# Kernel optimization log

Measured on AMD Instinct MI355X. Metric: run time of the kernel, lower is better.

## Reference

```python
import jax, jax.numpy as jnp
import numpy as np

NUM_NODES = 50000
NUM_HYPEREDGES = 10000
NUM_INCIDENCES = 800000
CHANNELS = 256
NEG_SLOPE = 0.01  # torch leaky_relu default negative_slope


def setup_inputs() -> dict:
    key = jax.random.key(0)
    k_n, k_e, k_emb, k_cw, k_lw, k_lb = jax.random.split(key, 6)
    node_idx = jax.random.randint(k_n, (NUM_INCIDENCES,), 0, NUM_NODES, dtype=jnp.int32)
    edge_idx = jax.random.randint(k_e, (NUM_INCIDENCES,), 0, NUM_HYPEREDGES, dtype=jnp.int32)
    edge_index = jnp.stack([node_idx, edge_idx], axis=0)  # [2, nnz] incidence list
    s = 1.0 / np.sqrt(CHANNELS).astype(np.float32)
    emb = jax.random.normal(k_emb, (NUM_NODES, CHANNELS), jnp.float32)  # Node2Vec embedding table
    conv_w = jax.random.normal(k_cw, (CHANNELS, CHANNELS), jnp.float32) * s  # HypergraphConv.lin (no bias)
    conv_b = jnp.zeros((CHANNELS,), jnp.float32)  # HypergraphConv.bias
    lin_w = jax.random.normal(k_lw, (CHANNELS, CHANNELS), jnp.float32) * s
    lin_b = jax.random.normal(k_lb, (CHANNELS,), jnp.float32) * s
    return {"emb": emb, "conv_w": conv_w, "conv_b": conv_b,
            "lin_w": lin_w, "lin_b": lin_b, "edge_index": edge_index}


def reference(emb, conv_w, conv_b, lin_w, lin_b, edge_index):
    node_idx, edge_idx = edge_index[0], edge_index[1]
    # HypergraphConv (use_attention=False): X' = D^-1 H B^-1 H^T (X W^T) + b
    x = emb @ conv_w.T  # [N, C]
    ones = jnp.ones((NUM_INCIDENCES,), x.dtype)
    D = jax.ops.segment_sum(ones, node_idx, num_segments=NUM_NODES)       # node degree
    Dinv = jnp.where(D > 0, 1.0 / D, 0.0)
    B = jax.ops.segment_sum(ones, edge_idx, num_segments=NUM_HYPEREDGES)  # hyperedge degree
    Binv = jnp.where(B > 0, 1.0 / B, 0.0)
    # node -> hyperedge aggregation
    e = jax.ops.segment_sum(x[node_idx], edge_idx, num_segments=NUM_HYPEREDGES) * Binv[:, None]  # [E, C]
    # hyperedge -> node aggregation
    n = jax.ops.segment_sum(e[edge_idx], node_idx, num_segments=NUM_NODES) * Dinv[:, None] + conv_b  # [N, C]
    y = jax.nn.leaky_relu(n, NEG_SLOPE)
    g = y.T @ y  # [C, C] Gram
    out = jax.nn.leaky_relu(g @ lin_w.T + lin_b, NEG_SLOPE)
    return out
```

## Files before the change

### kernel.cpp

```cpp
#include <hip/hip_runtime.h>

#define N_NODES 50000
#define N_EDGES 10000
#define NNZ     800000
#define C       256
#define SLOPE   0.01f
#define KTOT    50176
#define KCHUNK  512
#define NZB     98
#define MPAD    10048

#define NB      250
#define EB_E    40
#define EB_N    200
#define CHUNK   3125
#define CAP     6000
#define MP_E    288
#define MP_N    1408

#define EAGG_G  628
#define NAGG_G  1568

#define OFF_CC_E    0
#define OFF_CC_N    1024
#define OFF_CUR_E   2048
#define OFF_CUR_N   3072
#define OFF_DEG_E   4096
#define OFF_DEG_N   45056
#define ZERO_BYTES  245760
#define OFF_CB_E    266240
#define OFF_CB_N    267264
#define OFF_RS_N    268288
#define OFF_RS_E    468480
#define OFF_BUF_E   508672
#define OFF_BUF_N   3708672
#define OFF_CSR_E   6908672
#define OFF_CSR_N   10108672
#define OFF_EMBH    13308672
#define OFF_YT      13308672
#define OFF_EACC    39000064
#define OFF_E2      44144640
#define OFF_CWH     49289216
#define OFF_PART    49420288

typedef __attribute__((ext_vector_type(8))) short short8;
typedef __attribute__((ext_vector_type(4))) float floatx4;

static __device__ __forceinline__ unsigned short f2bf(float f) {
    unsigned int u = __float_as_uint(f);
    u = (u + 0x7fffu + ((u >> 16) & 1u)) >> 16;
    return (unsigned short)u;
}

static __device__ __forceinline__ void acc_bf8(const uint4 d, float* a) {
    a[0] += __uint_as_float(d.x << 16);
    a[1] += __uint_as_float(d.x & 0xffff0000u);
    a[2] += __uint_as_float(d.y << 16);
    a[3] += __uint_as_float(d.y & 0xffff0000u);
    a[4] += __uint_as_float(d.z << 16);
    a[5] += __uint_as_float(d.z & 0xffff0000u);
    a[6] += __uint_as_float(d.w << 16);
    a[7] += __uint_as_float(d.w & 0xffff0000u);
}

static __device__ __forceinline__ void idx8(const uint4 pk, int* ix) {
    ix[0] = (int)(pk.x & 0xffffu); ix[1] = (int)(pk.x >> 16);
    ix[2] = (int)(pk.y & 0xffffu); ix[3] = (int)(pk.y >> 16);
    ix[4] = (int)(pk.z & 0xffffu); ix[5] = (int)(pk.z >> 16);
    ix[6] = (int)(pk.w & 0xffffu); ix[7] = (int)(pk.w >> 16);
}

__global__ __launch_bounds__(256) void zero_kernel(float4* __restrict__ p, int n4) {
    int i = blockIdx.x * 256 + threadIdx.x;
    if (i < n4) p[i] = make_float4(0.f, 0.f, 0.f, 0.f);
}

#define PREP_EMB_BLOCKS 6251
#define PREP_CW_BLOCKS  32
__global__ __launch_bounds__(256) void prep_kernel(const float4* __restrict__ emb4,
                                                   uint4* __restrict__ embh4,
                                                   const float4* __restrict__ cw4,
                                                   uint4* __restrict__ cwh4,
                                                   const int* __restrict__ node_idx,
                                                   const int* __restrict__ edge_idx,
                                                   int* __restrict__ cc_e,
                                                   int* __restrict__ cc_n) {
    __shared__ int he[NB], hn[NB];
    int b = blockIdx.x, tid = threadIdx.x;
    if (b < PREP_EMB_BLOCKS) {
        int i = b * 256 + tid;
        if (i >= 1600032) return;
        uint4 o = {0u, 0u, 0u, 0u};
        if (i < 1600000) {
            float4 f0 = emb4[2 * i], f1 = emb4[2 * i + 1];
            o.x = f2bf(f0.x) | ((unsigned)f2bf(f0.y) << 16);
            o.y = f2bf(f0.z) | ((unsigned)f2bf(f0.w) << 16);
            o.z = f2bf(f1.x) | ((unsigned)f2bf(f1.y) << 16);
            o.w = f2bf(f1.z) | ((unsigned)f2bf(f1.w) << 16);
        }
        int node = i >> 5, c = i & 31;
        embh4[(size_t)(((c >> 2) * 50001 + node) << 2) + (c & 3)] = o;
    } else if (b < PREP_EMB_BLOCKS + PREP_CW_BLOCKS) {
        int i = (b - PREP_EMB_BLOCKS) * 256 + tid;
        float4 f0 = cw4[2 * i], f1 = cw4[2 * i + 1];
        uint4 o;
        o.x = f2bf(f0.x) | ((unsigned)f2bf(f0.y) << 16);
        o.y = f2bf(f0.z) | ((unsigned)f2bf(f0.w) << 16);
        o.z = f2bf(f1.x) | ((unsigned)f2bf(f1.y) << 16);
        o.w = f2bf(f1.z) | ((unsigned)f2bf(f1.w) << 16);
        cwh4[i] = o;
    } else {
        int base = (b - PREP_EMB_BLOCKS - PREP_CW_BLOCKS) * CHUNK;
        for (int i = tid; i < NB; i += 256) { he[i] = 0; hn[i] = 0; }
        __syncthreads();
        for (int i = tid; i < CHUNK; i += 256) {
            atomicAdd(&he[edge_idx[base + i] / EB_E], 1);
            atomicAdd(&hn[node_idx[base + i] / EB_N], 1);
        }
        __syncthreads();
        for (int k = tid; k < NB; k += 256) {
            if (he[k]) atomicAdd(&cc_e[k], he[k]);
            if (hn[k]) atomicAdd(&cc_n[k], hn[k]);
        }
    }
}

__global__ __launch_bounds__(256) void coarse_scan_kernel(const int* __restrict__ cc_e,
                                                          const int* __restrict__ cc_n,
                                                          int* __restrict__ cb_e,
                                                          int* __restrict__ cb_n) {
    __shared__ int tmp[256];
    int tid = threadIdx.x;
    int v = (tid < NB) ? cc_e[tid] : 0;
    tmp[tid] = v;
    __syncthreads();
    for (int off = 1; off < 256; off <<= 1) {
        int t = (tid >= off) ? tmp[tid - off] : 0;
        __syncthreads();
        tmp[tid] += t;
        __syncthreads();
    }
    if (tid < NB) cb_e[tid + 1] = tmp[tid];
    if (tid == 0) cb_e[0] = 0;
    __syncthreads();
    v = (tid < NB) ? cc_n[tid] : 0;
    tmp[tid] = v;
    __syncthreads();
    for (int off = 1; off < 256; off <<= 1) {
        int t = (tid >= off) ? tmp[tid - off] : 0;
        __syncthreads();
        tmp[tid] += t;
        __syncthreads();
    }
    if (tid < NB) cb_n[tid + 1] = tmp[tid];
    if (tid == 0) cb_n[0] = 0;
}

__global__ __launch_bounds__(256) void bucket_scatter_kernel(const int* __restrict__ node_idx,
                                                             const int* __restrict__ edge_idx,
                                                             const int* __restrict__ cb_e,
                                                             const int* __restrict__ cb_n,
                                                             int* __restrict__ cur_e,
                                                             int* __restrict__ cur_n,
                                                             int* __restrict__ buf_e,
                                                             int* __restrict__ buf_n) {
    __shared__ int he[NB], hn[NB], be[NB], bn[NB];
    int tid = threadIdx.x;
    int base = blockIdx.x * CHUNK;
    for (int i = tid; i < NB; i += 256) { he[i] = 0; hn[i] = 0; }
    __syncthreads();
    int pe[13], pn[13];
    #pragma unroll
    for (int k = 0; k < 13; k++) {
        int i = tid + k * 256;
        if (i < CHUNK) {
            int e = edge_idx[base + i], v = node_idx[base + i];
            int ke = e / EB_E, kn = v / EB_N;
            pe[k] = (ke << 12) | atomicAdd(&he[ke], 1);
            pn[k] = (kn << 12) | atomicAdd(&hn[kn], 1);
        }
    }
    __syncthreads();
    for (int k = tid; k < NB; k += 256) {
        int c = he[k];
        be[k] = cb_e[k] + (c ? atomicAdd(&cur_e[k], c) : 0);
        int cn = hn[k];
        bn[k] = cb_n[k] + (cn ? atomicAdd(&cur_n[k], cn) : 0);
    }
    __syncthreads();
    #pragma unroll
    for (int k = 0; k < 13; k++) {
        int i = tid + k * 256;
        if (i < CHUNK) {
            int e = edge_idx[base + i], v = node_idx[base + i];
            int ke = pe[k] >> 12, oe = pe[k] & 4095;
            buf_e[be[ke] + oe] = (v << 6) | (e - ke * EB_E);
            int kn = pn[k] >> 12, on = pn[k] & 4095;
            buf_n[bn[kn] + on] = (e << 8) | (v - kn * EB_N);
        }
    }
}

__global__ __launch_bounds__(256) void bucket_sort_kernel(const int* __restrict__ buf_e,
                                                          const int* __restrict__ buf_n,
                                                          const int* __restrict__ cb_e,
                                                          const int* __restrict__ cb_n,
                                                          unsigned short* __restrict__ csr_e,
                                                          unsigned short* __restrict__ csr_n,
                                                          int* __restrict__ rs_e,
                                                          int* __restrict__ rs_n,
                                                          int* __restrict__ deg_e,
                                                          int* __restrict__ deg_n) {
    __shared__ int A[CAP];
    __shared__ int h[EB_N], bs[EB_N], cs[EB_N];
    int tid = threadIdx.x;
    bool edgeSide = blockIdx.x < NB;
    int k = edgeSide ? blockIdx.x : blockIdx.x - NB;
    int eb = edgeSide ? EB_E : EB_N;
    int shift = edgeSide ? 6 : 8;
    int mask = (1 << shift) - 1;
    int mp = edgeSide ? MP_E : MP_N;
    int sent = edgeSide ? N_NODES : N_EDGES;
    const int* cb  = edgeSide ? cb_e : cb_n;
    const int* buf = edgeSide ? buf_e : buf_n;
    unsigned short* csr = edgeSide ? csr_e : csr_n;
    int* rs  = edgeSide ? rs_e : rs_n;
    int* deg = edgeSide ? deg_e : deg_n;
    int base = cb[k];
    int base_pad = (base + k * mp + 7) & ~7;
    int cnt = cb[k + 1] - base;
    for (int i = tid; i < eb; i += 256) h[i] = 0;
    __syncthreads();
    for (int i = tid; i < cnt; i += 256) {
        int it = buf[base + i];
        if (i < CAP) A[i] = it;
        atomicAdd(&h[it & mask], 1);
    }
    __syncthreads();
    if (tid == 0) {
        int s = 0;
        for (int j = 0; j < eb; j++) { bs[j] = s; s += (h[j] + 7) & ~7; }
    }
    __syncthreads();
    for (int j = tid; j < eb; j += 256) {
        rs[k * eb + j] = base_pad + bs[j];
        deg[k * eb + j] = h[j];
        cs[j] = h[j];
        h[j] = 0;
    }
    if (tid == 0 && k == NB - 1) rs[edgeSide ? N_EDGES : N_NODES] = NNZ;
    __syncthreads();
    for (int j = tid; j < eb; j += 256) {
        int c0 = cs[j], e0 = (c0 + 7) & ~7;
        for (int x = c0; x < e0; x++) csr[base_pad + bs[j] + x] = (unsigned short)sent;
    }
    for (int i = tid; i < cnt; i += 256) {
        int it = (i < CAP) ? A[i] : buf[base + i];
        int loc = it & mask;
        int off = bs[loc] + atomicAdd(&h[loc], 1);
        csr[base_pad + off] = (unsigned short)(it >> shift);
    }
}

__global__ __launch_bounds__(256) void edge_aggregate_kernel(const uint4* __restrict__ embh4,
                                                             const unsigned short* __restrict__ csr_e,
                                                             const int* __restrict__ rs_e,
                                                             const int* __restrict__ deg_e,
                                                             unsigned short* __restrict__ e_acc_h) {
    int sid = blockIdx.x & 7, g = blockIdx.x >> 3;
    const uint4* __restrict__ tbl = embh4 + (size_t)sid * 50001 * 4;
    const uint4* __restrict__ csr4 = (const uint4*)csr_e;
    int tid = threadIdx.x;
    int w = tid >> 6, lane = tid & 63;
    int grp = lane >> 4, q = (lane >> 2) & 3, c4 = lane & 3;
    int e = g * 16 + w * 4 + grp;
    int s = rs_e[e];
    int dg = deg_e[e];
    int c0 = s >> 3, nc = (dg + 7) >> 3;
    float a[8] = {0.f, 0.f, 0.f, 0.f, 0.f, 0.f, 0.f, 0.f};
    for (int c = c0 + q; c < c0 + nc; c += 4) {
        uint4 pk = csr4[c];
        int ix[8];
        idx8(pk, ix);
        #pragma unroll
        for (int j = 0; j < 8; j++) acc_bf8(tbl[ix[j] * 4 + c4], a);
    }
    #pragma unroll
    for (int off = 4; off <= 8; off <<= 1) {
        #pragma unroll
        for (int jj = 0; jj < 8; jj++) a[jj] += __shfl_xor(a[jj], off);
    }
    if (q == 0) {
        uint4 o;
        o.x = f2bf(a[0]) | ((unsigned)f2bf(a[1]) << 16);
        o.y = f2bf(a[2]) | ((unsigned)f2bf(a[3]) << 16);
        o.z = f2bf(a[4]) | ((unsigned)f2bf(a[5]) << 16);
        o.w = f2bf(a[6]) | ((unsigned)f2bf(a[7]) << 16);
        ((uint4*)(e_acc_h + (size_t)e * C + sid * 32))[c4] = o;
    }
}

__global__ __launch_bounds__(256) void edge_gemm_mfma_kernel(const unsigned short* __restrict__ e_acc_h,
                                                             const unsigned short* __restrict__ cwh,
                                                             const int* __restrict__ deg_e,
                                                             unsigned short* __restrict__ e2h) {
    __shared__ __align__(16) unsigned short As[64 * 72];
    __shared__ __align__(16) unsigned short Bs[64 * 72];
    int i0 = blockIdx.x * 64, j0 = blockIdx.y * 64;
    int tid = threadIdx.x;
    int w = tid >> 6, lane = tid & 63;
    int col = lane & 15, quad = lane >> 4;
    floatx4 acc[4] = {};
    for (int step = 0; step < 4; step++) {
        int kb = step * 64;
        __syncthreads();
        #pragma unroll
        for (int l = 0; l < 2; l++) {
            int slot = tid + l * 256;
            int row = slot >> 3, grp = slot & 7;
            uint4 da = *(const uint4*)(e_acc_h + (size_t)(i0 + row) * C + kb + grp * 8);
            *(uint4*)(&As[row * 72 + grp * 8]) = da;
            uint4 db = *(const uint4*)(cwh + (size_t)(j0 + row) * C + kb + grp * 8);
            *(uint4*)(&Bs[row * 72 + grp * 8]) = db;
        }
        __syncthreads();
        #pragma unroll
        for (int sub = 0; sub < 2; sub++) {
            short8 a = *(const short8*)(&As[(w * 16 + col) * 72 + sub * 32 + quad * 8]);
            #pragma unroll
            for (int jt = 0; jt < 4; jt++) {
                short8 b = *(const short8*)(&Bs[(jt * 16 + col) * 72 + sub * 32 + quad * 8]);
                acc[jt] = __builtin_amdgcn_mfma_f32_16x16x32_bf16(a, b, acc[jt], 0, 0, 0);
            }
        }
    }
    #pragma unroll
    for (int r = 0; r < 4; r++) {
        int m = i0 + w * 16 + quad * 4 + r;
        int dg = deg_e[m];
        float binv = (dg > 0) ? 1.0f / (float)dg : 0.0f;
        #pragma unroll
        for (int jt = 0; jt < 4; jt++) {
            int ch = j0 + jt * 16 + col;
            e2h[(size_t)((ch >> 6) * MPAD + m) * 64 + (ch & 63)] = f2bf(acc[jt][r] * binv);
        }
    }
}

__global__ __launch_bounds__(256) void node_aggregate_t_kernel(const uint4* __restrict__ e2h4,
                                                               const unsigned short* __restrict__ csr_n,
                                                               const int* __restrict__ rs_n,
                                                               const int* __restrict__ deg_n,
                                                               const float* __restrict__ conv_b,
                                                               unsigned short* __restrict__ yT) {
    __shared__ unsigned short T[64][33];
    int sid = blockIdx.x & 3, g = blockIdx.x >> 2;
    const uint4* __restrict__ csr4 = (const uint4*)csr_n;
    int tid = threadIdx.x;
    int group = tid >> 3, l8 = tid & 7;
    const uint4* __restrict__ tbl = e2h4 + (size_t)sid * MPAD * 8 + l8;
    int n = g * 32 + group;
    int s = rs_n[min(n, N_NODES)];
    int dg = deg_n[n];
    int c0 = s >> 3, nc = (dg + 7) >> 3;
    float4 b0 = ((const float4*)conv_b)[sid * 16 + l8 * 2];
    float4 b1 = ((const float4*)conv_b)[sid * 16 + l8 * 2 + 1];
    float a[8] = {0.f, 0.f, 0.f, 0.f, 0.f, 0.f, 0.f, 0.f};
    for (int c = c0; c < c0 + nc; c++) {
        uint4 pk = csr4[c];
        int ix[8];
        idx8(pk, ix);
        #pragma unroll
        for (int j = 0; j < 8; j++) acc_bf8(tbl[(size_t)ix[j] * 8], a);
    }
    float dinv = (dg > 0) ? 1.0f / (float)dg : 0.0f;
    float bb[8] = {b0.x, b0.y, b0.z, b0.w, b1.x, b1.y, b1.z, b1.w};
    #pragma unroll
    for (int jj = 0; jj < 8; jj++) {
        float r = a[jj] * dinv + bb[jj];
        r = (r > 0.f) ? r : SLOPE * r;
        if (n >= N_NODES) r = 0.f;
        T[l8 * 8 + jj][group] = f2bf(r);
    }
    __syncthreads();
    int rr = tid >> 2, cc = tid & 3;
    uint4 o;
    o.x = T[rr][cc * 8 + 0] | ((unsigned)T[rr][cc * 8 + 1] << 16);
    o.y = T[rr][cc * 8 + 2] | ((unsigned)T[rr][cc * 8 + 3] << 16);
    o.z = T[rr][cc * 8 + 4] | ((unsigned)T[rr][cc * 8 + 5] << 16);
    o.w = T[rr][cc * 8 + 6] | ((unsigned)T[rr][cc * 8 + 7] << 16);
    *(uint4*)(yT + (size_t)(sid * 64 + rr) * KTOT + g * 32 + cc * 8) = o;
}

__global__ __launch_bounds__(256) void gram_mfma_kernel(const unsigned short* __restrict__ yT,
                                                        float* __restrict__ part) {
    static const int PI[10] = {0, 0, 0, 0, 1, 1, 1, 2, 2, 3};
    static const int PJ[10] = {0, 1, 2, 3, 1, 2, 3, 2, 3, 3};
    __shared__ __align__(16) unsigned short As[64 * 72];
    __shared__ __align__(16) unsigned short Bs[64 * 72];
    int i0 = PI[blockIdx.x] * 64, j0 = PJ[blockIdx.x] * 64;
    bool diag = (i0 == j0);
    int kb0 = blockIdx.y * KCHUNK;
    int tid = threadIdx.x;
    int w = tid >> 6, lane = tid & 63;
    int col = lane & 15, quad = lane >> 4;
    floatx4 acc[4] = {};
    for (int step = 0; step < KCHUNK / 64; step++) {
        int kb = kb0 + step * 64;
        __syncthreads();
        #pragma unroll
        for (int l = 0; l < 2; l++) {
            int slot = tid + l * 256;
            int row = slot >> 3, grp = slot & 7;
            uint4 da = *(const uint4*)(yT + (size_t)(i0 + row) * KTOT + kb + grp * 8);
            *(uint4*)(&As[row * 72 + grp * 8]) = da;
            if (!diag) {
                uint4 db = *(const uint4*)(yT + (size_t)(j0 + row) * KTOT + kb + grp * 8);
                *(uint4*)(&Bs[row * 72 + grp * 8]) = db;
            }
        }
        __syncthreads();
        const unsigned short* Bb = diag ? As : Bs;
        #pragma unroll
        for (int sub = 0; sub < 2; sub++) {
            short8 a = *(const short8*)(&As[(w * 16 + col) * 72 + sub * 32 + quad * 8]);
            #pragma unroll
            for (int jt = 0; jt < 4; jt++) {
                short8 b = *(const short8*)(&Bb[(jt * 16 + col) * 72 + sub * 32 + quad * 8]);
                acc[jt] = __builtin_amdgcn_mfma_f32_16x16x32_bf16(a, b, acc[jt], 0, 0, 0);
            }
        }
    }
    float* slab = part + ((size_t)blockIdx.y * 10 + blockIdx.x) * 4096;
    #pragma unroll
    for (int jt = 0; jt < 4; jt++)
        #pragma unroll
        for (int r = 0; r < 4; r++)
            slab[(w * 16 + quad * 4 + r) * 64 + jt * 16 + col] = acc[jt][r];
}

__global__ __launch_bounds__(256) void greduce_out_kernel(const float* __restrict__ part,
                                                          const float* __restrict__ lin_w,
                                                          const float* __restrict__ lin_b,
                                                          float* __restrict__ out) {
    __shared__ float gs[C];
    int i = blockIdx.x, j = threadIdx.x;
    int a = i >> 6, b = j >> 6;
    int lo = min(a, b), hi = max(a, b);
    int t = lo * (7 - lo) / 2 + hi;
    int li = (a <= b) ? (i & 63) : (j & 63);
    int lj = (a <= b) ? (j & 63) : (i & 63);
    const float* p = part + (size_t)t * 4096 + li * 64 + lj;
    float s = 0.f;
    for (int z = 0; z < NZB; z++) s += p[(size_t)z * 40960];
    gs[j] = s;
    __syncthreads();
    float acc = lin_b[j];
    const float* wrow = lin_w + (size_t)j * C;
    for (int k = 0; k < C; k++) acc += gs[k] * wrow[k];
    out[(size_t)i * C + j] = (acc > 0.f) ? acc : SLOPE * acc;
}

extern "C" void kernel_launch(void* const* d_in, const int* in_sizes, int n_in,
                              void* d_out, int out_size, void* d_ws, size_t ws_size,
                              hipStream_t stream) {
    const float* emb    = (const float*)d_in[0];
    const float* conv_w = (const float*)d_in[1];
    const float* conv_b = (const float*)d_in[2];
    const float* lin_w  = (const float*)d_in[3];
    const float* lin_b  = (const float*)d_in[4];
    const int*   eidx   = (const int*)d_in[5];
    const int* node_idx = eidx;
    const int* edge_idx = eidx + NNZ;

    char* ws = (char*)d_ws;
    int* cc_e  = (int*)(ws + OFF_CC_E);
    int* cc_n  = (int*)(ws + OFF_CC_N);
    int* cur_e = (int*)(ws + OFF_CUR_E);
    int* cur_n = (int*)(ws + OFF_CUR_N);
    int* deg_e = (int*)(ws + OFF_DEG_E);
    int* deg_n = (int*)(ws + OFF_DEG_N);
    int* cb_e  = (int*)(ws + OFF_CB_E);
    int* cb_n  = (int*)(ws + OFF_CB_N);
    int* rs_n  = (int*)(ws + OFF_RS_N);
    int* rs_e  = (int*)(ws + OFF_RS_E);
    int* buf_e = (int*)(ws + OFF_BUF_E);
    int* buf_n = (int*)(ws + OFF_BUF_N);
    unsigned short* csr_e = (unsigned short*)(ws + OFF_CSR_E);
    unsigned short* csr_n = (unsigned short*)(ws + OFF_CSR_N);
    uint4* embh4 = (uint4*)(ws + OFF_EMBH);
    unsigned short* e_acc_h = (unsigned short*)(ws + OFF_EACC);
    unsigned short* e2h = (unsigned short*)(ws + OFF_E2);
    unsigned short* cwh = (unsigned short*)(ws + OFF_CWH);
    unsigned short* yT  = (unsigned short*)(ws + OFF_YT);
    float* part = (float*)(ws + OFF_PART);
    float* out = (float*)d_out;

    zero_kernel<<<ZERO_BYTES / 4096, 256, 0, stream>>>((float4*)ws, ZERO_BYTES / 16);

    prep_kernel<<<PREP_EMB_BLOCKS + PREP_CW_BLOCKS + 256, 256, 0, stream>>>(
        (const float4*)emb, embh4, (const float4*)conv_w, (uint4*)cwh,
        node_idx, edge_idx, cc_e, cc_n);

    coarse_scan_kernel<<<1, 256, 0, stream>>>(cc_e, cc_n, cb_e, cb_n);

    bucket_scatter_kernel<<<256, 256, 0, stream>>>(node_idx, edge_idx, cb_e, cb_n,
                                                   cur_e, cur_n, buf_e, buf_n);

    bucket_sort_kernel<<<2 * NB, 256, 0, stream>>>(buf_e, buf_n, cb_e, cb_n,
                                                   csr_e, csr_n, rs_e, rs_n,
                                                   deg_e, deg_n);

    edge_aggregate_kernel<<<8 * EAGG_G, 256, 0, stream>>>(embh4, csr_e, rs_e, deg_e, e_acc_h);

    edge_gemm_mfma_kernel<<<dim3(MPAD / 64, C / 64), 256, 0, stream>>>(e_acc_h, cwh, deg_e, e2h);

    node_aggregate_t_kernel<<<4 * NAGG_G, 256, 0, stream>>>((const uint4*)e2h, csr_n, rs_n,
                                                            deg_n, conv_b, yT);

    gram_mfma_kernel<<<dim3(10, NZB), 256, 0, stream>>>(yT, part);

    greduce_out_kernel<<<C, 256, 0, stream>>>(part, lin_w, lin_b, out);
}
```

Measured before the change: 261.1 us.

## Split edge gather by node-range halves with wider channel slices, sum partials in GEMM

The embedding table is re-laid out in 64-channel slices, and the edge aggregation now splits work into two node-index halves times four channel slices. Each 8-lane group handles one edge sequentially and skips neighbours outside its half. The intent is to shrink the gathered table footprint per block so it fits better in cache, at the cost of scanning every CSR entry twice. The two bf16 partial sums are added while the edge GEMM loads its tiles, which adds an extra rounding step and extra load traffic there.

```diff
diff --git a/kernel.cpp b/kernel.cpp
--- a/kernel.cpp
+++ b/kernel.cpp
@@ -9,6 +9,7 @@
 #define KCHUNK  512
 #define NZB     98
 #define MPAD    10048
+#define NHALF   25000
 
 #define NB      250
 #define EB_E    40
@@ -18,7 +19,7 @@
 #define MP_E    288
 #define MP_N    1408
 
-#define EAGG_G  628
+#define EAGG_G  314
 #define NAGG_G  1568
 
 #define OFF_CC_E    0
@@ -38,10 +39,10 @@
 #define OFF_CSR_N   10108672
 #define OFF_EMBH    13308672
 #define OFF_YT      13308672
-#define OFF_EACC    39000064
 #define OFF_E2      44144640
 #define OFF_CWH     49289216
 #define OFF_PART    49420288
+#define OFF_EACCP   OFF_PART
 
 typedef __attribute__((ext_vector_type(8))) short short8;
 typedef __attribute__((ext_vector_type(4))) float floatx4;
@@ -68,6 +69,17 @@
     ix[2] = (int)(pk.y & 0xffffu); ix[3] = (int)(pk.y >> 16);
     ix[4] = (int)(pk.z & 0xffffu); ix[5] = (int)(pk.z >> 16);
     ix[6] = (int)(pk.w & 0xffffu); ix[7] = (int)(pk.w >> 16);
+}
+
+static __device__ __forceinline__ unsigned bfadd2(unsigned x, unsigned y) {
+    float lx = __uint_as_float(x << 16), hx = __uint_as_float(x & 0xffff0000u);
+    float ly = __uint_as_float(y << 16), hy = __uint_as_float(y & 0xffff0000u);
+    return (unsigned)f2bf(lx + ly) | ((unsigned)f2bf(hx + hy) << 16);
+}
+static __device__ __forceinline__ uint4 bfadd8(uint4 x, uint4 y) {
+    x.x = bfadd2(x.x, y.x); x.y = bfadd2(x.y, y.y);
+    x.z = bfadd2(x.z, y.z); x.w = bfadd2(x.w, y.w);
+    return x;
 }
 
 __global__ __launch_bounds__(256) void zero_kernel(float4* __restrict__ p, int n4) {
@@ -99,7 +111,7 @@
             o.w = f2bf(f1.z) | ((unsigned)f2bf(f1.w) << 16);
         }
         int node = i >> 5, c = i & 31;
-        embh4[(size_t)(((c >> 2) * 50001 + node) << 2) + (c & 3)] = o;
+        embh4[((size_t)(c >> 3) * 50001 + node) * 8 + (c & 7)] = o;
     } else if (b < PREP_EMB_BLOCKS + PREP_CW_BLOCKS) {
         int i = (b - PREP_EMB_BLOCKS) * 256 + tid;
         float4 f0 = cw4[2 * i], f1 = cw4[2 * i + 1];
@@ -266,41 +278,39 @@
                                                              const unsigned short* __restrict__ csr_e,
                                                              const int* __restrict__ rs_e,
                                                              const int* __restrict__ deg_e,
-                                                             unsigned short* __restrict__ e_acc_h) {
+                                                             unsigned short* __restrict__ e_accp) {
     int sid = blockIdx.x & 7, g = blockIdx.x >> 3;
-    const uint4* __restrict__ tbl = embh4 + (size_t)sid * 50001 * 4;
+    int cslice = sid & 3, half = sid >> 2;
+    int lo = half * NHALF, hi = lo + NHALF;
     const uint4* __restrict__ csr4 = (const uint4*)csr_e;
     int tid = threadIdx.x;
-    int w = tid >> 6, lane = tid & 63;
-    int grp = lane >> 4, q = (lane >> 2) & 3, c4 = lane & 3;
-    int e = g * 16 + w * 4 + grp;
-    int s = rs_e[e];
+    int group = tid >> 3, l8 = tid & 7;
+    const uint4* __restrict__ tbl = embh4 + (size_t)cslice * 50001 * 8 + l8;
+    int e = g * 32 + group;
+    int s = rs_e[min(e, N_EDGES)];
     int dg = deg_e[e];
     int c0 = s >> 3, nc = (dg + 7) >> 3;
     float a[8] = {0.f, 0.f, 0.f, 0.f, 0.f, 0.f, 0.f, 0.f};
-    for (int c = c0 + q; c < c0 + nc; c += 4) {
+    for (int c = c0; c < c0 + nc; c++) {
         uint4 pk = csr4[c];
         int ix[8];
         idx8(pk, ix);
         #pragma unroll
-        for (int j = 0; j < 8; j++) acc_bf8(tbl[ix[j] * 4 + c4], a);
-    }
-    #pragma unroll
-    for (int off = 4; off <= 8; off <<= 1) {
-        #pragma unroll
-        for (int jj = 0; jj < 8; jj++) a[jj] += __shfl_xor(a[jj], off);
-    }
-    if (q == 0) {
-        uint4 o;
-        o.x = f2bf(a[0]) | ((unsigned)f2bf(a[1]) << 16);
-        o.y = f2bf(a[2]) | ((unsigned)f2bf(a[3]) << 16);
-        o.z = f2bf(a[4]) | ((unsigned)f2bf(a[5]) << 16);
-        o.w = f2bf(a[6]) | ((unsigned)f2bf(a[7]) << 16);
-        ((uint4*)(e_acc_h + (size_t)e * C + sid * 32))[c4] = o;
-    }
-}
-
-__global__ __launch_bounds__(256) void edge_gemm_mfma_kernel(const unsigned short* __restrict__ e_acc_h,
+        for (int j = 0; j < 8; j++) {
+            int v = ix[j];
+            if (v >= lo && v < hi)
+                acc_bf8(tbl[(size_t)v * 8], a);
+        }
+    }
+    uint4 o;
+    o.x = f2bf(a[0]) | ((unsigned)f2bf(a[1]) << 16);
+    o.y = f2bf(a[2]) | ((unsigned)f2bf(a[3]) << 16);
+    o.z = f2bf(a[4]) | ((unsigned)f2bf(a[5]) << 16);
+    o.w = f2bf(a[6]) | ((unsigned)f2bf(a[7]) << 16);
+    *(uint4*)(e_accp + ((size_t)half * MPAD + e) * C + cslice * 64 + l8 * 8) = o;
+}
+
+__global__ __launch_bounds__(256) void edge_gemm_mfma_kernel(const unsigned short* __restrict__ e_accp,
                                                              const unsigned short* __restrict__ cwh,
                                                              const int* __restrict__ deg_e,
                                                              unsigned short* __restrict__ e2h) {
@@ -318,8 +328,9 @@
         for (int l = 0; l < 2; l++) {
             int slot = tid + l * 256;
             int row = slot >> 3, grp = slot & 7;
-            uint4 da = *(const uint4*)(e_acc_h + (size_t)(i0 + row) * C + kb + grp * 8);
-            *(uint4*)(&As[row * 72 + grp * 8]) = da;
+            uint4 d0 = *(const uint4*)(e_accp + (size_t)(i0 + row) * C + kb + grp * 8);
+            uint4 d1 = *(const uint4*)(e_accp + ((size_t)MPAD + i0 + row) * C + kb + grp * 8);
+            *(uint4*)(&As[row * 72 + grp * 8]) = bfadd8(d0, d1);
             uint4 db = *(const uint4*)(cwh + (size_t)(j0 + row) * C + kb + grp * 8);
             *(uint4*)(&Bs[row * 72 + grp * 8]) = db;
         }
@@ -489,7 +500,7 @@
     unsigned short* csr_e = (unsigned short*)(ws + OFF_CSR_E);
     unsigned short* csr_n = (unsigned short*)(ws + OFF_CSR_N);
     uint4* embh4 = (uint4*)(ws + OFF_EMBH);
-    unsigned short* e_acc_h = (unsigned short*)(ws + OFF_EACC);
+    unsigned short* e_accp = (unsigned short*)(ws + OFF_EACCP);
     unsigned short* e2h = (unsigned short*)(ws + OFF_E2);
     unsigned short* cwh = (unsigned short*)(ws + OFF_CWH);
     unsigned short* yT  = (unsigned short*)(ws + OFF_YT);
@@ -511,9 +522,9 @@
                                                    csr_e, csr_n, rs_e, rs_n,
                                                    deg_e, deg_n);
 
-    edge_aggregate_kernel<<<8 * EAGG_G, 256, 0, stream>>>(embh4, csr_e, rs_e, deg_e, e_acc_h);
-
-    edge_gemm_mfma_kernel<<<dim3(MPAD / 64, C / 64), 256, 0, stream>>>(e_acc_h, cwh, deg_e, e2h);
+    edge_aggregate_kernel<<<8 * EAGG_G, 256, 0, stream>>>(embh4, csr_e, rs_e, deg_e, e_accp);
+
+    edge_gemm_mfma_kernel<<<dim3(MPAD / 64, C / 64), 256, 0, stream>>>(e_accp, cwh, deg_e, e2h);
 
     node_aggregate_t_kernel<<<4 * NAGG_G, 256, 0, stream>>>((const uint4*)e2h, csr_n, rs_n,
                                                             deg_n, conv_b, yT);
```

After: 299.3 us. 1.15x slower.
